# Optimization experiments

Hardware: AMD Instinct MI355X
Metric: run time of the kernel (lower is better)

## Reference

```python
import jax, jax.numpy as jnp
import numpy as np

B, N, DIM, HID, MAXN = 2048, 65536, 256, 512, 64
MID_KEY = (MAXN + HID) // 2   # 288
MID_VAL = (DIM + HID) // 2    # 384
MID_DEC = (HID + DIM) // 2    # 384
MID_SZ  = (HID + 1) // 2      # 256

def _ln(x, g, b):
    m = x.mean(-1, keepdims=True)
    v = ((x - m) ** 2).mean(-1, keepdims=True)
    return (x - m) * jax.lax.rsqrt(v + 1e-5) * g + b

def _mish(x):
    return x * jnp.tanh(jax.nn.softplus(x))

def _mlp_ln(x, W1, b1, g, be, W2, b2):
    return _mish(_ln(x @ W1 + b1, g, be)) @ W2 + b2

def _mlp(x, W1, b1, W2, b2):
    return _mish(x @ W1 + b1) @ W2 + b2

def setup_inputs():
    key = jax.random.key(0)
    ks = iter(jax.random.split(key, 40))
    def rn(shape, s=0.05):
        return jax.random.normal(next(ks), shape, jnp.float32) * s
    x = jax.random.normal(next(ks), (N, DIM), jnp.float32)
    batch = jnp.sort(jax.random.randint(next(ks), (N,), 0, B)).astype(jnp.int32)
    z32 = lambda *s: jnp.zeros(s, jnp.float32)
    o32 = lambda *s: jnp.ones(s, jnp.float32)
    return dict(
        x=x, batch=batch, n_batches=B,
        e_rank_W=rn((DIM, 1)), e_rank_b=z32(1),
        e_card_W=rn((1, HID)), e_card_b=z32(HID),
        e_key_W1=rn((MAXN, MID_KEY)), e_key_b1=z32(MID_KEY), e_key_g=o32(MID_KEY), e_key_be=z32(MID_KEY),
        e_key_W2=rn((MID_KEY, HID)), e_key_b2=z32(HID),
        e_val_W1=rn((DIM, MID_VAL)), e_val_b1=z32(MID_VAL), e_val_g=o32(MID_VAL), e_val_be=z32(MID_VAL),
        e_val_W2=rn((MID_VAL, HID)), e_val_b2=z32(HID),
        d_key_W1=rn((MAXN, MID_KEY)), d_key_b1=z32(MID_KEY), d_key_g=o32(MID_KEY), d_key_be=z32(MID_KEY),
        d_key_W2=rn((MID_KEY, HID)), d_key_b2=z32(HID),
        d_dec_W1=rn((HID, MID_DEC)), d_dec_b1=z32(MID_DEC),
        d_dec_W2=rn((MID_DEC, DIM)), d_dec_b2=z32(DIM),
        d_size_W1=rn((HID, MID_SZ)), d_size_b1=z32(MID_SZ), d_size_g=o32(MID_SZ), d_size_be=z32(MID_SZ),
        d_size_W2=rn((MID_SZ, 1)), d_size_b2=z32(1),
    )

def reference(x, batch, n_batches, e_rank_W, e_rank_b, e_card_W, e_card_b,
              e_key_W1, e_key_b1, e_key_g, e_key_be, e_key_W2, e_key_b2,
              e_val_W1, e_val_b1, e_val_g, e_val_be, e_val_W2, e_val_b2,
              d_key_W1, d_key_b1, d_key_g, d_key_be, d_key_W2, d_key_b2,
              d_dec_W1, d_dec_b1, d_dec_W2, d_dec_b2,
              d_size_W1, d_size_b1, d_size_g, d_size_be, d_size_W2, d_size_b2):
    max_n = e_key_W1.shape[0]
    n_pts = x.shape[0]
    # ---- Encoder ----
    n = jax.ops.segment_sum(jnp.ones(n_pts, jnp.float32), batch, num_segments=n_batches).astype(jnp.int32)
    mag = jnp.abs(x @ e_rank_W + e_rank_b)[:, 0]                 # [N]
    sort_key = batch.astype(jnp.float32) * jnp.max(mag) + mag    # sort within each set by |rank|
    idx = jnp.argsort(sort_key)
    xs = x[idx]
    starts = jnp.cumsum(n) - n                                   # per-set offsets (batch is sorted)
    pos_idx = jnp.arange(n_pts) - starts[batch]                  # rank within each set
    pos = jax.nn.one_hot(pos_idx, max_n, dtype=x.dtype)
    y = _mlp_ln(xs, e_val_W1, e_val_b1, e_val_g, e_val_be, e_val_W2, e_val_b2) \
      * _mlp_ln(pos, e_key_W1, e_key_b1, e_key_g, e_key_be, e_key_W2, e_key_b2)
    z = jax.ops.segment_sum(y, batch, num_segments=n_batches) \
      + n.astype(jnp.float32)[:, None] @ e_card_W + e_card_b     # [B, HID]
    # ---- Decoder ----
    n_logits = _mlp_ln(z, d_size_W1, d_size_b1, d_size_g, d_size_be, d_size_W2, d_size_b2)  # [B, 1]
    n_dec = jnp.clip(jnp.round(n_logits[:, 0]), 0, max_n).astype(jnp.int32)
    keys = _mlp_ln(jnp.eye(max_n, dtype=x.dtype),                # onehot positions 0..max_n-1
                   d_key_W1, d_key_b1, d_key_g, d_key_be, d_key_W2, d_key_b2)  # [max_n, HID]
    zp = z[:, None, :] * keys[None, :, :]                        # [B, max_n, HID] (repeat_interleave -> dense+mask)
    xf = _mlp(zp, d_dec_W1, d_dec_b1, d_dec_W2, d_dec_b2)        # [B, max_n, DIM]
    mask = jnp.arange(max_n)[None, :] < n_dec[:, None]           # valid rows per set
    x_out = (xf * mask[..., None].astype(xf.dtype)).reshape(-1, xf.shape[-1])
    batch_out = jnp.repeat(jnp.arange(n_batches, dtype=jnp.int32), max_n)
    return x_out, batch_out, mask.reshape(-1)
```

## Files before the change

kernel.cpp:

```cpp
#include <hip/hip_runtime.h>

#define NPTS   65536
#define NB     2048
#define DIMX   256
#define HIDN   512
#define MAXNN  64
#define MIDK   288
#define MIDV   384
#define MIDD   384
#define MIDS   256

typedef unsigned short ushort_t;
typedef __attribute__((ext_vector_type(8))) short short8;
typedef __attribute__((ext_vector_type(4))) float f32x4;

__device__ __forceinline__ float mishf(float x) {
    float e = __expf(fminf(x, 30.f));
    float n = e * (e + 2.f);
    return x * n * __builtin_amdgcn_rcpf(n + 2.f);
}
__device__ __forceinline__ ushort_t f2bf(float f) {
    unsigned u = __float_as_uint(f);
    u += 0x7fffu + ((u >> 16) & 1u);
    return (ushort_t)(u >> 16);
}
__device__ __forceinline__ float bf2f(ushort_t h) {
    return __uint_as_float(((unsigned)h) << 16);
}
__device__ __forceinline__ void dma16(const void* g, void* lds) {
    __builtin_amdgcn_global_load_lds(
        (const __attribute__((address_space(1))) unsigned int*)g,
        (__attribute__((address_space(3))) unsigned int*)lds, 16, 0, 0);
}

__global__ __launch_bounds__(256)
void k_starts(const int* __restrict__ batch, int* __restrict__ starts,
              unsigned int* __restrict__ maxmag, int* __restrict__ cnt)
{
    int b = blockIdx.x * blockDim.x + threadIdx.x;
    if (b == 0) { *maxmag = 0u; *cnt = 0; }
    if (b <= NB) {
        int lo = 0, hi = NPTS;
        while (lo < hi) { int mid = (lo + hi) >> 1; if (batch[mid] < b) lo = mid + 1; else hi = mid; }
        starts[b] = lo;
    }
}

__global__ __launch_bounds__(256)
void k_mag(const float* __restrict__ x, const float* __restrict__ rW,
           const float* __restrict__ rb, float* __restrict__ mag,
           unsigned int* __restrict__ maxmag, ushort_t* __restrict__ xb)
{
    const int lane = threadIdx.x & 63;
    const int wave = threadIdx.x >> 6;
    const int gw = blockIdx.x * 4 + wave;
    float4 wv = *(const float4*)(rW + lane * 4);
    float bias = rb[0];
    float lmax = 0.f;
    for (int pt = gw; pt < NPTS; pt += 16384) {
        float4 xv = *(const float4*)(x + (size_t)pt * DIMX + lane * 4);
        ushort4 u;
        u.x = f2bf(xv.x); u.y = f2bf(xv.y); u.z = f2bf(xv.z); u.w = f2bf(xv.w);
        *(ushort4*)(xb + (size_t)pt * DIMX + lane * 4) = u;
        double d = (double)xv.x * wv.x + (double)xv.y * wv.y
                 + (double)xv.z * wv.z + (double)xv.w * wv.w;
        #pragma unroll
        for (int o = 32; o > 0; o >>= 1) d += __shfl_xor(d, o);
        float s = fabsf((float)(d + (double)bias));
        if (lane == 0) mag[pt] = s;
        lmax = fmaxf(lmax, s);
    }
    __shared__ float wm[4];
    if (lane == 0) wm[wave] = lmax;
    __syncthreads();
    if (threadIdx.x == 0) {
        float m = fmaxf(fmaxf(wm[0], wm[1]), fmaxf(wm[2], wm[3]));
        atomicMax(maxmag, __float_as_uint(m));
    }
}

__global__ __launch_bounds__(256)
void k_rank(const int* __restrict__ batch, const int* __restrict__ starts,
            const float* __restrict__ mag, const unsigned int* __restrict__ maxmag,
            int* __restrict__ kidx)
{
    int i = blockIdx.x * 256 + threadIdx.x;
    if (i >= NPTS) return;
    int b = batch[i];
    int s = starts[b], e = starts[b + 1];
    float M = __uint_as_float(*maxmag);
    float kb = __fmul_rn((float)b, M);
    float ki = __fadd_rn(kb, mag[i]);
    int r = 0;
    for (int j = s; j < e; ++j) {
        float kj = __fadd_rn(kb, mag[j]);
        r += (kj < ki) || (kj == ki && j < i);
    }
    kidx[i] = (r < MAXNN) ? r : MAXNN;
}

__global__ __launch_bounds__(512)
void k_table(const float* __restrict__ W1, const float* __restrict__ b1,
             const float* __restrict__ g, const float* __restrict__ be,
             const float* __restrict__ W2, const float* __restrict__ b2,
             float* __restrict__ tbl, int in_dim, int n_w1_rows)
{
    const int row = blockIdx.x;
    const int t = threadIdx.x;
    __shared__ float h[MIDK];
    __shared__ float red[512];
    float v = 0.f;
    if (t < in_dim) v = b1[t] + (row < n_w1_rows ? W1[row * in_dim + t] : 0.f);
    red[t] = (t < in_dim) ? v : 0.f;
    __syncthreads();
    for (int o = 256; o > 0; o >>= 1) { if (t < o) red[t] += red[t + o]; __syncthreads(); }
    float m = red[0] / (float)in_dim;
    __syncthreads();
    float d = v - m;
    red[t] = (t < in_dim) ? d * d : 0.f;
    __syncthreads();
    for (int o = 256; o > 0; o >>= 1) { if (t < o) red[t] += red[t + o]; __syncthreads(); }
    float rs = rsqrtf(red[0] / (float)in_dim + 1e-5f);
    __syncthreads();
    if (t < in_dim) h[t] = mishf(d * rs * g[t] + be[t]);
    __syncthreads();
    float acc = b2[t];
    #pragma unroll 8
    for (int k = 0; k < MIDK; ++k) acc = fmaf(h[k], W2[k * HIDN + t], acc);
    tbl[row * HIDN + t] = acc;
}

__global__ __launch_bounds__(256)
void k_card(const int* __restrict__ starts, const float* __restrict__ cardW,
            const float* __restrict__ cardb, float* __restrict__ z)
{
    int idx = blockIdx.x * 256 + threadIdx.x;
    int b = idx >> 9, c = idx & 511;
    float n = (float)(starts[b + 1] - starts[b]);
    z[idx] = fmaf(n, cardW[c], cardb[c]);
}

__global__ __launch_bounds__(256)
void k_size(const float* __restrict__ z, const float* __restrict__ W1,
            const float* __restrict__ b1, const float* __restrict__ g,
            const float* __restrict__ be, const float* __restrict__ W2,
            const float* __restrict__ b2, int* __restrict__ ndec)
{
    const int b0 = blockIdx.x * 4, t = threadIdx.x;
    __shared__ float zr[4][HIDN];
    __shared__ float red[4][256];
    #pragma unroll
    for (int gI = 0; gI < 4; ++gI) {
        zr[gI][t] = z[(b0 + gI) * HIDN + t];
        zr[gI][t + 256] = z[(b0 + gI) * HIDN + 256 + t];
    }
    __syncthreads();
    float acc[4];
    float bb1 = b1[t];
    #pragma unroll
    for (int gI = 0; gI < 4; ++gI) acc[gI] = bb1;
    #pragma unroll 8
    for (int k = 0; k < HIDN; ++k) {
        float wv = W1[k * MIDS + t];
        #pragma unroll
        for (int gI = 0; gI < 4; ++gI) acc[gI] = fmaf(zr[gI][k], wv, acc[gI]);
    }
    #pragma unroll
    for (int gI = 0; gI < 4; ++gI) red[gI][t] = acc[gI];
    __syncthreads();
    for (int o = 128; o > 0; o >>= 1) {
        if (t < o) {
            #pragma unroll
            for (int gI = 0; gI < 4; ++gI) red[gI][t] += red[gI][t + o];
        }
        __syncthreads();
    }
    float mm[4];
    #pragma unroll
    for (int gI = 0; gI < 4; ++gI) mm[gI] = red[gI][0] * (1.f / 256.f);
    __syncthreads();
    #pragma unroll
    for (int gI = 0; gI < 4; ++gI) { float d = acc[gI] - mm[gI]; red[gI][t] = d * d; }
    __syncthreads();
    for (int o = 128; o > 0; o >>= 1) {
        if (t < o) {
            #pragma unroll
            for (int gI = 0; gI < 4; ++gI) red[gI][t] += red[gI][t + o];
        }
        __syncthreads();
    }
    float rs[4];
    #pragma unroll
    for (int gI = 0; gI < 4; ++gI) rs[gI] = rsqrtf(red[gI][0] * (1.f / 256.f) + 1e-5f);
    __syncthreads();
    float w2 = W2[t], gg = g[t], bbe = be[t];
    #pragma unroll
    for (int gI = 0; gI < 4; ++gI) {
        float h = mishf((acc[gI] - mm[gI]) * rs[gI] * gg + bbe);
        red[gI][t] = h * w2;
    }
    __syncthreads();
    for (int o = 128; o > 0; o >>= 1) {
        if (t < o) {
            #pragma unroll
            for (int gI = 0; gI < 4; ++gI) red[gI][t] += red[gI][t + o];
        }
        __syncthreads();
    }
    if (t < 4) {
        float logit = red[t][0] + b2[0];
        float n = rintf(logit);
        n = fminf(fmaxf(n, 0.f), 64.f);
        ndec[b0 + t] = (int)n;
    }
}

__global__ __launch_bounds__(256)
void k_compact(const int* __restrict__ ndec, int* __restrict__ cnt,
               int* __restrict__ rowmap)
{
    int b = blockIdx.x * 256 + threadIdx.x;
    if (b >= NB) return;
    int n = ndec[b];
    if (n > 0) {
        int base = atomicAdd(cnt, n);
        for (int p = 0; p < n; ++p) rowmap[base + p] = b * 64 + p;
    }
}

__global__ __launch_bounds__(128)
void k_pad(const int* __restrict__ cnt, int* __restrict__ cntpad,
           int* __restrict__ rowmap)
{
    int c = *cnt;
    int pad = (c + 127) & ~127;
    int t = threadIdx.x;
    if (c + t < pad) rowmap[c + t] = -1;
    if (t == 0) *cntpad = pad;
}

__global__ __launch_bounds__(256)
void k_tail(const int* __restrict__ ndec, float* __restrict__ outb,
            float* __restrict__ outm)
{
    int r = blockIdx.x * 256 + threadIdx.x;
    if (r < NB * MAXNN) {
        outb[r] = (float)(r >> 6);
        outm[r] = ((r & 63) < ndec[r >> 6]) ? 1.f : 0.f;
    }
}

__global__ __launch_bounds__(256)
void k_wt_all(const float* __restrict__ W0, ushort_t* __restrict__ T0,
              const float* __restrict__ W1s, ushort_t* __restrict__ T1,
              const float* __restrict__ W2s, ushort_t* __restrict__ T2,
              const float* __restrict__ W3s, ushort_t* __restrict__ T3)
{
    int idx = blockIdx.x * 256 + threadIdx.x;
    const float* W; ushort_t* T; int N, K, off;
    if (idx < 98304)       { W = W0;  T = T0; K = 256; N = 384; off = idx; }
    else if (idx < 294912) { W = W1s; T = T1; K = 384; N = 512; off = idx - 98304; }
    else if (idx < 491520) { W = W2s; T = T2; K = 512; N = 384; off = idx - 294912; }
    else                   { W = W3s; T = T3; K = 384; N = 256; off = idx - 491520; }
    int k = off / N, n = off - k * N;
    T[(size_t)n * K + k] = f2bf(W[off]);
}

__global__ __launch_bounds__(512, 2)
void k_mm_e1f(const ushort_t* __restrict__ A, const ushort_t* __restrict__ Bt,
              const float* __restrict__ bias, const float* __restrict__ g,
              const float* __restrict__ be, ushort_t* __restrict__ C)
{
    const int m0 = blockIdx.x * 128;
    __shared__ __align__(16) ushort_t As[128 * 64];
    __shared__ __align__(16) ushort_t Bs[384 * 64];
    const int t = threadIdx.x;
    const int l = t & 63;
    const int w = t >> 6;
    const int wm = (w >> 2) * 64;
    const int wq = (w & 3) * 96;
    const int l4 = (l >> 4) << 2;
    const int drow = l >> 3;
    const int dblk = (l & 7) ^ drow;

    f32x4 acc[4][6];
    #pragma unroll
    for (int a = 0; a < 4; ++a)
        #pragma unroll
        for (int b = 0; b < 6; ++b) acc[a][b] = (f32x4)0.f;

    for (int k0 = 0; k0 < DIMX; k0 += 64) {
        #pragma unroll
        for (int ii = 0; ii < 2; ++ii) {
            int i = w * 2 + ii;
            dma16(A + (size_t)(m0 + i * 8 + drow) * DIMX + k0 + dblk * 8, &As[i * 512]);
        }
        #pragma unroll
        for (int ii = 0; ii < 6; ++ii) {
            int i = w * 6 + ii;
            dma16(Bt + (size_t)(i * 8 + drow) * DIMX + k0 + dblk * 8, &Bs[i * 512]);
        }
        __syncthreads();
        #pragma unroll
        for (int ks = 0; ks < 2; ++ks) {
            int kq = ks * 4 + (l >> 4);
            short8 af[4], bfr[6];
            #pragma unroll
            for (int fm = 0; fm < 4; ++fm) {
                int row = wm + fm * 16 + (l & 15);
                af[fm] = *(const short8*)&As[row * 64 + ((kq ^ (row & 7)) << 3)];
            }
            #pragma unroll
            for (int fn = 0; fn < 6; ++fn) {
                int row = wq + fn * 16 + (l & 15);
                bfr[fn] = *(const short8*)&Bs[row * 64 + ((kq ^ (row & 7)) << 3)];
            }
            #pragma unroll
            for (int fm = 0; fm < 4; ++fm)
                #pragma unroll
                for (int fn = 0; fn < 6; ++fn)
                    acc[fm][fn] = __builtin_amdgcn_mfma_f32_16x16x32_bf16(
                        af[fm], bfr[fn], acc[fm][fn], 0, 0, 0);
        }
        __syncthreads();
    }

    float bb[6], gg[6], bee[6];
    #pragma unroll
    for (int fn = 0; fn < 6; ++fn) {
        int col = wq + fn * 16 + (l & 15);
        bb[fn] = bias[col]; gg[fn] = g[col]; bee[fn] = be[col];
    }
    #pragma unroll
    for (int fm = 0; fm < 4; ++fm)
        #pragma unroll
        for (int fn = 0; fn < 6; ++fn)
            #pragma unroll
            for (int j = 0; j < 4; ++j) acc[fm][fn][j] += bb[fn];

    float* ssum = (float*)As;
    float* ssq  = ssum + 512;
    #pragma unroll
    for (int fm = 0; fm < 4; ++fm) {
        #pragma unroll
        for (int j = 0; j < 4; ++j) {
            float s = 0.f, q = 0.f;
            #pragma unroll
            for (int fn = 0; fn < 6; ++fn) {
                float v = acc[fm][fn][j];
                s += v; q += v * v;
            }
            #pragma unroll
            for (int o = 1; o < 16; o <<= 1) {
                s += __shfl_xor(s, o);
                q += __shfl_xor(q, o);
            }
            if ((l & 15) == 0) {
                int r = wm + fm * 16 + l4 + j;
                ssum[r * 4 + (w & 3)] = s;
                ssq[r * 4 + (w & 3)] = q;
            }
        }
    }
    __syncthreads();
    #pragma unroll
    for (int fm = 0; fm < 4; ++fm) {
        #pragma unroll
        for (int j = 0; j < 4; ++j) {
            int r = wm + fm * 16 + l4 + j;
            float s = ssum[r * 4 + 0] + ssum[r * 4 + 1] + ssum[r * 4 + 2] + ssum[r * 4 + 3];
            float q = ssq[r * 4 + 0] + ssq[r * 4 + 1] + ssq[r * 4 + 2] + ssq[r * 4 + 3];
            float m = s * (1.f / 384.f);
            float var = q * (1.f / 384.f) - m * m;
            float rs = rsqrtf(var + 1e-5f);
            #pragma unroll
            for (int fn = 0; fn < 6; ++fn) {
                float v = (acc[fm][fn][j] - m) * rs * gg[fn] + bee[fn];
                C[(size_t)(m0 + r) * MIDV + wq + fn * 16 + (l & 15)] = f2bf(mishf(v));
            }
        }
    }
}

template<int MODE>
__device__ __forceinline__
void mm_body(const ushort_t* __restrict__ A, const ushort_t* __restrict__ Bt,
             const float* __restrict__ bias, void* __restrict__ Cptr, int K,
             const float* __restrict__ tbl, const int* __restrict__ kidx,
             const int* __restrict__ batch, float* __restrict__ zout,
             const float* __restrict__ zin, const int* __restrict__ rowmap,
             const int* __restrict__ cntpad)
{
    const int flat = blockIdx.y * gridDim.x + blockIdx.x;
    const int nx = gridDim.x;
    const int xcd = flat & 7;
    const int lin = flat >> 3;
    const int n0 = (lin % nx) * 128;
    const int m0 = ((lin / nx) + ((gridDim.y >> 3) * xcd)) * 128;
    if (MODE >= 2) {
        if (m0 >= *cntpad) return;
    }
    __shared__ __align__(16) ushort_t sAB[2 * 128 * 64];
    ushort_t* As = sAB;
    ushort_t* Bs = sAB + 128 * 64;
    const int t = threadIdx.x;
    const int l = t & 63;
    const int w = t >> 6;
    const int wm = (w >> 1) * 64;
    const int wn = (w & 1) * 64;
    const int l4 = (l >> 4) << 2;
    const int drow = l >> 3;
    const int dblk = (l & 7) ^ drow;

    int g4[4], p4[4];
    if (MODE == 2) {
        #pragma unroll
        for (int ii = 0; ii < 4; ++ii) {
            int i = w * 4 + ii;
            int gr = rowmap[m0 + i * 8 + drow];
            if (gr < 0) gr = 0;
            g4[ii] = gr >> 6; p4[ii] = gr & 63;
        }
    }

    f32x4 acc[4][4];
    #pragma unroll
    for (int a = 0; a < 4; ++a)
        #pragma unroll
        for (int b = 0; b < 4; ++b) acc[a][b] = (f32x4)0.f;

    for (int k0 = 0; k0 < K; k0 += 64) {
        if (MODE == 2) {
            #pragma unroll
            for (int ii = 0; ii < 4; ++ii) {
                int i = w * 4 + ii;
                int row = i * 8 + drow;
                const float* zp = zin + g4[ii] * HIDN + k0 + dblk * 8;
                const float* kp = tbl + p4[ii] * HIDN + k0 + dblk * 8;
                float4 z0 = *(const float4*)zp;
                float4 z1 = *(const float4*)(zp + 4);
                float4 q0 = *(const float4*)kp;
                float4 q1 = *(const float4*)(kp + 4);
                ushort4 u0, u1;
                u0.x = f2bf(z0.x * q0.x); u0.y = f2bf(z0.y * q0.y);
                u0.z = f2bf(z0.z * q0.z); u0.w = f2bf(z0.w * q0.w);
                u1.x = f2bf(z1.x * q1.x); u1.y = f2bf(z1.y * q1.y);
                u1.z = f2bf(z1.z * q1.z); u1.w = f2bf(z1.w * q1.w);
                ushort_t* dst = &As[row * 64 + (l & 7) * 8];
                *(ushort4*)dst = u0;
                *(ushort4*)(dst + 4) = u1;
            }
        } else {
            #pragma unroll
            for (int ii = 0; ii < 4; ++ii) {
                int i = w * 4 + ii;
                const ushort_t* g = A + (size_t)(m0 + i * 8 + drow) * K + k0 + dblk * 8;
                dma16(g, &As[i * 512]);
            }
        }
        #pragma unroll
        for (int ii = 0; ii < 4; ++ii) {
            int i = w * 4 + ii;
            const ushort_t* g = Bt + (size_t)(n0 + i * 8 + drow) * K + k0 + dblk * 8;
            dma16(g, &Bs[i * 512]);
        }
        __syncthreads();
        #pragma unroll
        for (int ks = 0; ks < 2; ++ks) {
            short8 af[4], bfr[4];
            int kq = ks * 4 + (l >> 4);
            #pragma unroll
            for (int fm = 0; fm < 4; ++fm) {
                int row = wm + fm * 16 + (l & 15);
                af[fm] = *(const short8*)&As[row * 64 + ((kq ^ (row & 7)) << 3)];
            }
            #pragma unroll
            for (int fn = 0; fn < 4; ++fn) {
                int row = wn + fn * 16 + (l & 15);
                bfr[fn] = *(const short8*)&Bs[row * 64 + ((kq ^ (row & 7)) << 3)];
            }
            #pragma unroll
            for (int fm = 0; fm < 4; ++fm)
                #pragma unroll
                for (int fn = 0; fn < 4; ++fn)
                    acc[fm][fn] = __builtin_amdgcn_mfma_f32_16x16x32_bf16(
                        af[fm], bfr[fn], acc[fm][fn], 0, 0, 0);
        }
        __syncthreads();
    }

    if (MODE == 1) {
        __shared__ int barr[128];
        __shared__ int karr[128];
        float* yred = (float*)sAB;
        if (t < 128) { barr[t] = batch[m0 + t]; karr[t] = kidx[m0 + t]; }
        __syncthreads();
        #pragma unroll
        for (int pass = 0; pass < 2; ++pass) {
            if (wm == pass * 64) {
                #pragma unroll
                for (int fn = 0; fn < 4; ++fn) {
                    int cl = wn + fn * 16 + (l & 15);
                    float bb = bias[n0 + cl];
                    #pragma unroll
                    for (int fm = 0; fm < 4; ++fm) {
                        #pragma unroll
                        for (int j = 0; j < 4; ++j) {
                            int rl = fm * 16 + l4 + j;
                            float v = (acc[fm][fn][j] + bb)
                                    * tbl[karr[pass * 64 + rl] * HIDN + (n0 + cl)];
                            yred[cl * 64 + (rl ^ (cl & 31))] = v;
                        }
                    }
                }
            }
            __syncthreads();
            {
                int c = t & 127, half = t >> 7;
                int gc = n0 + c;
                float run = 0.f; int curb = -1;
                #pragma unroll 1
                for (int rr = 0; rr < 32; ++rr) {
                    int rl = half * 32 + rr;
                    int b = barr[pass * 64 + rl];
                    float v = yred[c * 64 + (rl ^ (c & 31))];
                    if (b != curb) {
                        if (curb >= 0) atomicAdd(&zout[curb * HIDN + gc], run);
                        curb = b; run = v;
                    } else run += v;
                }
                atomicAdd(&zout[curb * HIDN + gc], run);
            }
            __syncthreads();
        }
    } else if (MODE == 2) {
        ushort_t* C = (ushort_t*)Cptr;
        #pragma unroll
        for (int fm = 0; fm < 4; ++fm) {
            int gr0 = m0 + wm + fm * 16 + l4;
            #pragma unroll
            for (int fn = 0; fn < 4; ++fn) {
                int gc = n0 + wn + fn * 16 + (l & 15);
                float bb = bias[gc];
                #pragma unroll
                for (int j = 0; j < 4; ++j)
                    C[(size_t)(gr0 + j) * MIDD + gc] = f2bf(mishf(acc[fm][fn][j] + bb));
            }
        }
    } else if (MODE == 3) {
        float* C = (float*)Cptr;
        #pragma unroll
        for (int fm = 0; fm < 4; ++fm) {
            int gr0 = m0 + wm + fm * 16 + l4;
            int om[4];
            #pragma unroll
            for (int j = 0; j < 4; ++j) om[j] = rowmap[gr0 + j];
            #pragma unroll
            for (int fn = 0; fn < 4; ++fn) {
                int gc = n0 + wn + fn * 16 + (l & 15);
                float bb = bias[gc];
                #pragma unroll
                for (int j = 0; j < 4; ++j)
                    if (om[j] >= 0) C[(size_t)om[j] * DIMX + gc] = acc[fm][fn][j] + bb;
            }
        }
    }
}

__global__ __launch_bounds__(256, 2)
void k_mm_e2(const ushort_t* A, const ushort_t* Bt, const float* bias, int K,
             const float* tbl, const int* kidx, const int* batch, float* zout)
{ mm_body<1>(A, Bt, bias, nullptr, K, tbl, kidx, batch, zout, nullptr, nullptr, nullptr); }

__global__ __launch_bounds__(256, 2)
void k_mm_d1(const ushort_t* Bt, const float* bias, void* C, int K,
             const float* tbl, const float* zin, const int* rowmap, const int* cntpad)
{ mm_body<2>(nullptr, Bt, bias, C, K, tbl, nullptr, nullptr, nullptr, zin, rowmap, cntpad); }

__global__ __launch_bounds__(256, 2)
void k_mm_d2(const ushort_t* A, const ushort_t* Bt, const float* bias, void* C, int K,
             const int* rowmap, const int* cntpad)
{ mm_body<3>(A, Bt, bias, C, K, nullptr, nullptr, nullptr, nullptr, nullptr, rowmap, cntpad); }

extern "C" void kernel_launch(void* const* d_in, const int* in_sizes, int n_in,
                              void* d_out, int out_size, void* d_ws, size_t ws_size,
                              hipStream_t stream)
{
    const float* x        = (const float*)d_in[0];
    const int*   batch    = (const int*)  d_in[1];
    const float* e_rank_W = (const float*)d_in[3];
    const float* e_rank_b = (const float*)d_in[4];
    const float* e_card_W = (const float*)d_in[5];
    const float* e_card_b = (const float*)d_in[6];
    const float* e_key_W1 = (const float*)d_in[7];
    const float* e_key_b1 = (const float*)d_in[8];
    const float* e_key_g  = (const float*)d_in[9];
    const float* e_key_be = (const float*)d_in[10];
    const float* e_key_W2 = (const float*)d_in[11];
    const float* e_key_b2 = (const float*)d_in[12];
    const float* e_val_W1 = (const float*)d_in[13];
    const float* e_val_b1 = (const float*)d_in[14];
    const float* e_val_g  = (const float*)d_in[15];
    const float* e_val_be = (const float*)d_in[16];
    const float* e_val_W2 = (const float*)d_in[17];
    const float* e_val_b2 = (const float*)d_in[18];
    const float* d_key_W1 = (const float*)d_in[19];
    const float* d_key_b1 = (const float*)d_in[20];
    const float* d_key_g  = (const float*)d_in[21];
    const float* d_key_be = (const float*)d_in[22];
    const float* d_key_W2 = (const float*)d_in[23];
    const float* d_key_b2 = (const float*)d_in[24];
    const float* d_dec_W1 = (const float*)d_in[25];
    const float* d_dec_b1 = (const float*)d_in[26];
    const float* d_dec_W2 = (const float*)d_in[27];
    const float* d_dec_b2 = (const float*)d_in[28];
    const float* d_size_W1= (const float*)d_in[29];
    const float* d_size_b1= (const float*)d_in[30];
    const float* d_size_g = (const float*)d_in[31];
    const float* d_size_be= (const float*)d_in[32];
    const float* d_size_W2= (const float*)d_in[33];
    const float* d_size_b2= (const float*)d_in[34];

    char* ws = (char*)d_ws;
    int*          starts  = (int*)         (ws + 0);
    unsigned int* maxmag  = (unsigned int*)(ws + 8448);
    int*          kidx    = (int*)         (ws + 8704);
    float*        mag     = (float*)       (ws + 270848);
    float*        enc_tbl = (float*)       (ws + 532992);
    float*        dec_tbl = (float*)       (ws + 666112);
    float*        z       = (float*)       (ws + 797184);
    int*          ndec    = (int*)         (ws + 4991488);
    int*          cnt     = (int*)         (ws + 4999680);
    int*          cntpad  = (int*)         (ws + 4999684);
    int*          rowmap  = (int*)         (ws + 5000192);
    ushort_t*     evW1t   = (ushort_t*)    (ws + 5524480);
    ushort_t*     evW2t   = (ushort_t*)    (ws + 5721088);
    ushort_t*     ddW1t   = (ushort_t*)    (ws + 6114304);
    ushort_t*     ddW2t   = (ushort_t*)    (ws + 6507520);
    ushort_t*     xb      = (ushort_t*)    (ws + 6704384);
    ushort_t*     Hb      = (ushort_t*)    (ws + 6704384 + 33554432);
    ushort_t*     Hd      = (ushort_t*)    (ws + 6704384);

    float* out_x = (float*)d_out;
    float* out_b = out_x + (size_t)NB * MAXNN * DIMX;
    float* out_m = out_b + NB * MAXNN;

    hipMemsetAsync(out_x, 0, (size_t)NB * MAXNN * DIMX * sizeof(float), stream);
    k_starts<<<dim3(9), dim3(256), 0, stream>>>(batch, starts, maxmag, cnt);
    k_mag<<<dim3(4096), dim3(256), 0, stream>>>(x, e_rank_W, e_rank_b, mag, maxmag, xb);
    k_rank<<<dim3(256), dim3(256), 0, stream>>>(batch, starts, mag, maxmag, kidx);
    k_table<<<dim3(65), dim3(512), 0, stream>>>(e_key_W1, e_key_b1, e_key_g, e_key_be,
                                                e_key_W2, e_key_b2, enc_tbl, MIDK, 64);
    k_table<<<dim3(64), dim3(512), 0, stream>>>(d_key_W1, d_key_b1, d_key_g, d_key_be,
                                                d_key_W2, d_key_b2, dec_tbl, MIDK, 64);
    k_card<<<dim3(4096), dim3(256), 0, stream>>>(starts, e_card_W, e_card_b, z);
    k_wt_all<<<dim3(2304), dim3(256), 0, stream>>>(e_val_W1, evW1t, e_val_W2, evW2t,
                                                   d_dec_W1, ddW1t, d_dec_W2, ddW2t);

    k_mm_e1f<<<dim3(512), dim3(512), 0, stream>>>(xb, evW1t, e_val_b1,
                                                  e_val_g, e_val_be, Hb);
    k_mm_e2<<<dim3(4, 512), dim3(256), 0, stream>>>(Hb, evW2t, e_val_b2, MIDV,
                                                    enc_tbl, kidx, batch, z);
    k_size<<<dim3(NB / 4), dim3(256), 0, stream>>>(z, d_size_W1, d_size_b1, d_size_g,
                                                   d_size_be, d_size_W2, d_size_b2, ndec);
    k_compact<<<dim3(8), dim3(256), 0, stream>>>(ndec, cnt, rowmap);
    k_pad<<<dim3(1), dim3(128), 0, stream>>>(cnt, cntpad, rowmap);
    k_mm_d1<<<dim3(3, 1024), dim3(256), 0, stream>>>(ddW1t, d_dec_b1, Hd, HIDN,
                                                     dec_tbl, z, rowmap, cntpad);
    k_mm_d2<<<dim3(2, 1024), dim3(256), 0, stream>>>(Hd, ddW2t, d_dec_b2, out_x, MIDD,
                                                     rowmap, cntpad);
    k_tail<<<dim3(512), dim3(256), 0, stream>>>(ndec, out_b, out_m);
}
```

Measured before the change: 520.6 us.

## Fuse encoder value MLP GEMMs and merge small setup kernels

Fuses the two encoder value-MLP GEMMs into one kernel. The bf16 hidden activations stay in LDS, laid out as swizzled K-panels, instead of round-tripping a 65536x384 buffer through global memory. The second GEMM loops over four 128-column output tiles per block, reusing the resident hidden slab, and performs the key-table multiply and segment-sum atomics in the epilogue. It also merges the two key-table launches into one grid and replaces the compact and pad kernels with a single-block kernel using an LDS counter. The cost is about 129 KB of LDS per block, which limits occupancy, and a serialized loop over output tiles within each block.

```diff
diff --git a/kernel.cpp b/kernel.cpp
--- a/kernel.cpp
+++ b/kernel.cpp
@@ -35,10 +35,10 @@
 
 __global__ __launch_bounds__(256)
 void k_starts(const int* __restrict__ batch, int* __restrict__ starts,
-              unsigned int* __restrict__ maxmag, int* __restrict__ cnt)
+              unsigned int* __restrict__ maxmag)
 {
     int b = blockIdx.x * blockDim.x + threadIdx.x;
-    if (b == 0) { *maxmag = 0u; *cnt = 0; }
+    if (b == 0) *maxmag = 0u;
     if (b <= NB) {
         int lo = 0, hi = NPTS;
         while (lo < hi) { int mid = (lo + hi) >> 1; if (batch[mid] < b) lo = mid + 1; else hi = mid; }
@@ -100,34 +100,46 @@
 }
 
 __global__ __launch_bounds__(512)
-void k_table(const float* __restrict__ W1, const float* __restrict__ b1,
-             const float* __restrict__ g, const float* __restrict__ be,
-             const float* __restrict__ W2, const float* __restrict__ b2,
-             float* __restrict__ tbl, int in_dim, int n_w1_rows)
+void k_table2(const float* __restrict__ eW1, const float* __restrict__ eb1,
+              const float* __restrict__ eg, const float* __restrict__ ebe,
+              const float* __restrict__ eW2, const float* __restrict__ eb2,
+              const float* __restrict__ dW1, const float* __restrict__ db1,
+              const float* __restrict__ dg, const float* __restrict__ dbe,
+              const float* __restrict__ dW2, const float* __restrict__ db2,
+              float* __restrict__ enc_tbl, float* __restrict__ dec_tbl)
 {
     const int row = blockIdx.x;
     const int t = threadIdx.x;
+    const float *W1, *b1, *g, *be, *W2, *b2; float* out; int wrow;
+    if (row < 65) {
+        W1 = eW1; b1 = eb1; g = eg; be = ebe; W2 = eW2; b2 = eb2;
+        out = enc_tbl + row * HIDN; wrow = (row < 64) ? row : -1;
+    } else {
+        int r = row - 65;
+        W1 = dW1; b1 = db1; g = dg; be = dbe; W2 = dW2; b2 = db2;
+        out = dec_tbl + r * HIDN; wrow = r;
+    }
     __shared__ float h[MIDK];
     __shared__ float red[512];
     float v = 0.f;
-    if (t < in_dim) v = b1[t] + (row < n_w1_rows ? W1[row * in_dim + t] : 0.f);
-    red[t] = (t < in_dim) ? v : 0.f;
+    if (t < MIDK) v = b1[t] + (wrow >= 0 ? W1[wrow * MIDK + t] : 0.f);
+    red[t] = (t < MIDK) ? v : 0.f;
     __syncthreads();
     for (int o = 256; o > 0; o >>= 1) { if (t < o) red[t] += red[t + o]; __syncthreads(); }
-    float m = red[0] / (float)in_dim;
+    float m = red[0] / (float)MIDK;
     __syncthreads();
     float d = v - m;
-    red[t] = (t < in_dim) ? d * d : 0.f;
+    red[t] = (t < MIDK) ? d * d : 0.f;
     __syncthreads();
     for (int o = 256; o > 0; o >>= 1) { if (t < o) red[t] += red[t + o]; __syncthreads(); }
-    float rs = rsqrtf(red[0] / (float)in_dim + 1e-5f);
-    __syncthreads();
-    if (t < in_dim) h[t] = mishf(d * rs * g[t] + be[t]);
+    float rs = rsqrtf(red[0] / (float)MIDK + 1e-5f);
+    __syncthreads();
+    if (t < MIDK) h[t] = mishf(d * rs * g[t] + be[t]);
     __syncthreads();
     float acc = b2[t];
     #pragma unroll 8
     for (int k = 0; k < MIDK; ++k) acc = fmaf(h[k], W2[k * HIDN + t], acc);
-    tbl[row * HIDN + t] = acc;
+    out[t] = acc;
 }
 
 __global__ __launch_bounds__(256)
@@ -216,26 +228,24 @@
 }
 
 __global__ __launch_bounds__(256)
-void k_compact(const int* __restrict__ ndec, int* __restrict__ cnt,
-               int* __restrict__ rowmap)
-{
-    int b = blockIdx.x * 256 + threadIdx.x;
-    if (b >= NB) return;
-    int n = ndec[b];
-    if (n > 0) {
-        int base = atomicAdd(cnt, n);
-        for (int p = 0; p < n; ++p) rowmap[base + p] = b * 64 + p;
-    }
-}
-
-__global__ __launch_bounds__(128)
-void k_pad(const int* __restrict__ cnt, int* __restrict__ cntpad,
-           int* __restrict__ rowmap)
-{
-    int c = *cnt;
+void k_compact_pad(const int* __restrict__ ndec, int* __restrict__ rowmap,
+                   int* __restrict__ cntpad)
+{
+    __shared__ int lcnt;
+    const int t = threadIdx.x;
+    if (t == 0) lcnt = 0;
+    __syncthreads();
+    for (int b = t; b < NB; b += 256) {
+        int n = ndec[b];
+        if (n > 0) {
+            int base = atomicAdd(&lcnt, n);
+            for (int p = 0; p < n; ++p) rowmap[base + p] = b * 64 + p;
+        }
+    }
+    __syncthreads();
+    int c = lcnt;
     int pad = (c + 127) & ~127;
-    int t = threadIdx.x;
-    if (c + t < pad) rowmap[c + t] = -1;
+    for (int i = c + t; i < pad; i += 256) rowmap[i] = -1;
     if (t == 0) *cntpad = pad;
 }
 
@@ -267,22 +277,34 @@
 }
 
 __global__ __launch_bounds__(512, 2)
-void k_mm_e1f(const ushort_t* __restrict__ A, const ushort_t* __restrict__ Bt,
-              const float* __restrict__ bias, const float* __restrict__ g,
-              const float* __restrict__ be, ushort_t* __restrict__ C)
+void k_enc(const ushort_t* __restrict__ A, const ushort_t* __restrict__ B1t,
+           const float* __restrict__ b1, const float* __restrict__ g,
+           const float* __restrict__ be, const ushort_t* __restrict__ B2t,
+           const float* __restrict__ b2, const float* __restrict__ tbl,
+           const int* __restrict__ kidx, const int* __restrict__ batch,
+           float* __restrict__ zout)
 {
     const int m0 = blockIdx.x * 128;
-    __shared__ __align__(16) ushort_t As[128 * 64];
-    __shared__ __align__(16) ushort_t Bs[384 * 64];
+    __shared__ __align__(16) char SMEM[132096];
+    ushort_t* slab = (ushort_t*)SMEM;
+    ushort_t* As   = slab;
+    ushort_t* Bs   = slab + 8192;
+    ushort_t* Bs2  = (ushort_t*)(SMEM + 98304);
+    float*    yred = (float*)(SMEM + 98304);
+    float*    ssum = (float*)(SMEM + 98304);
+    float*    ssq  = ssum + 512;
+    int*      barr = (int*)(SMEM + 131072);
+    int*      karr = barr + 128;
+
     const int t = threadIdx.x;
     const int l = t & 63;
     const int w = t >> 6;
-    const int wm = (w >> 2) * 64;
-    const int wq = (w & 3) * 96;
     const int l4 = (l >> 4) << 2;
     const int drow = l >> 3;
     const int dblk = (l & 7) ^ drow;
 
+    const int wmA = (w >> 2) * 64;
+    const int wqA = (w & 3) * 96;
     f32x4 acc[4][6];
     #pragma unroll
     for (int a = 0; a < 4; ++a)
@@ -298,7 +320,7 @@
         #pragma unroll
         for (int ii = 0; ii < 6; ++ii) {
             int i = w * 6 + ii;
-            dma16(Bt + (size_t)(i * 8 + drow) * DIMX + k0 + dblk * 8, &Bs[i * 512]);
+            dma16(B1t + (size_t)(i * 8 + drow) * DIMX + k0 + dblk * 8, &Bs[i * 512]);
         }
         __syncthreads();
         #pragma unroll
@@ -307,12 +329,12 @@
             short8 af[4], bfr[6];
             #pragma unroll
             for (int fm = 0; fm < 4; ++fm) {
-                int row = wm + fm * 16 + (l & 15);
+                int row = wmA + fm * 16 + (l & 15);
                 af[fm] = *(const short8*)&As[row * 64 + ((kq ^ (row & 7)) << 3)];
             }
             #pragma unroll
             for (int fn = 0; fn < 6; ++fn) {
-                int row = wq + fn * 16 + (l & 15);
+                int row = wqA + fn * 16 + (l & 15);
                 bfr[fn] = *(const short8*)&Bs[row * 64 + ((kq ^ (row & 7)) << 3)];
             }
             #pragma unroll
@@ -328,8 +350,8 @@
     float bb[6], gg[6], bee[6];
     #pragma unroll
     for (int fn = 0; fn < 6; ++fn) {
-        int col = wq + fn * 16 + (l & 15);
-        bb[fn] = bias[col]; gg[fn] = g[col]; bee[fn] = be[col];
+        int col = wqA + fn * 16 + (l & 15);
+        bb[fn] = b1[col]; gg[fn] = g[col]; bee[fn] = be[col];
     }
     #pragma unroll
     for (int fm = 0; fm < 4; ++fm)
@@ -338,8 +360,6 @@
             #pragma unroll
             for (int j = 0; j < 4; ++j) acc[fm][fn][j] += bb[fn];
 
-    float* ssum = (float*)As;
-    float* ssq  = ssum + 512;
     #pragma unroll
     for (int fm = 0; fm < 4; ++fm) {
         #pragma unroll
@@ -356,18 +376,20 @@
                 q += __shfl_xor(q, o);
             }
             if ((l & 15) == 0) {
-                int r = wm + fm * 16 + l4 + j;
+                int r = wmA + fm * 16 + l4 + j;
                 ssum[r * 4 + (w & 3)] = s;
                 ssq[r * 4 + (w & 3)] = q;
             }
         }
     }
-    __syncthreads();
+    if (t < 128) { barr[t] = batch[m0 + t]; karr[t] = kidx[m0 + t]; }
+    __syncthreads();
+
     #pragma unroll
     for (int fm = 0; fm < 4; ++fm) {
         #pragma unroll
         for (int j = 0; j < 4; ++j) {
-            int r = wm + fm * 16 + l4 + j;
+            int r = wmA + fm * 16 + l4 + j;
             float s = ssum[r * 4 + 0] + ssum[r * 4 + 1] + ssum[r * 4 + 2] + ssum[r * 4 + 3];
             float q = ssq[r * 4 + 0] + ssq[r * 4 + 1] + ssq[r * 4 + 2] + ssq[r * 4 + 3];
             float m = s * (1.f / 384.f);
@@ -376,8 +398,98 @@
             #pragma unroll
             for (int fn = 0; fn < 6; ++fn) {
                 float v = (acc[fm][fn][j] - m) * rs * gg[fn] + bee[fn];
-                C[(size_t)(m0 + r) * MIDV + wq + fn * 16 + (l & 15)] = f2bf(mishf(v));
-            }
+                int c = wqA + fn * 16 + (l & 15);
+                int panel = c >> 6, cc = c & 63;
+                int kb = (cc >> 3) ^ (r & 7);
+                slab[panel * 8192 + r * 64 + kb * 8 + (cc & 7)] = f2bf(mishf(v));
+            }
+        }
+    }
+    __syncthreads();
+
+    const int wmB = (w >> 1) * 32;
+    const int wnB = (w & 1) * 64;
+    for (int nt = 0; nt < 4; ++nt) {
+        const int n0t = nt * 128;
+        f32x4 acc2[2][4];
+        #pragma unroll
+        for (int a = 0; a < 2; ++a)
+            #pragma unroll
+            for (int b = 0; b < 4; ++b) acc2[a][b] = (f32x4)0.f;
+
+        for (int k0 = 0; k0 < MIDV; k0 += 64) {
+            const int panel = k0 >> 6;
+            #pragma unroll
+            for (int ii = 0; ii < 2; ++ii) {
+                int i = w * 2 + ii;
+                dma16(B2t + (size_t)(n0t + i * 8 + drow) * MIDV + k0 + dblk * 8,
+                      &Bs2[i * 512]);
+            }
+            __syncthreads();
+            #pragma unroll
+            for (int ks = 0; ks < 2; ++ks) {
+                int kq = ks * 4 + (l >> 4);
+                short8 af[2], bfr[4];
+                #pragma unroll
+                for (int fm = 0; fm < 2; ++fm) {
+                    int row = wmB + fm * 16 + (l & 15);
+                    af[fm] = *(const short8*)&slab[panel * 8192 + row * 64
+                                                   + ((kq ^ (row & 7)) << 3)];
+                }
+                #pragma unroll
+                for (int fn = 0; fn < 4; ++fn) {
+                    int row = wnB + fn * 16 + (l & 15);
+                    bfr[fn] = *(const short8*)&Bs2[row * 64 + ((kq ^ (row & 7)) << 3)];
+                }
+                #pragma unroll
+                for (int fm = 0; fm < 2; ++fm)
+                    #pragma unroll
+                    for (int fn = 0; fn < 4; ++fn)
+                        acc2[fm][fn] = __builtin_amdgcn_mfma_f32_16x16x32_bf16(
+                            af[fm], bfr[fn], acc2[fm][fn], 0, 0, 0);
+            }
+            __syncthreads();
+        }
+
+        #pragma unroll
+        for (int ph = 0; ph < 2; ++ph) {
+            if ((w >> 2) == ph) {
+                int rowbase = ((w >> 1) & 1) * 32;
+                #pragma unroll
+                for (int fn = 0; fn < 4; ++fn) {
+                    int cl = wnB + fn * 16 + (l & 15);
+                    float bbv = b2[n0t + cl];
+                    #pragma unroll
+                    for (int fm = 0; fm < 2; ++fm) {
+                        #pragma unroll
+                        for (int j = 0; j < 4; ++j) {
+                            int rl = rowbase + fm * 16 + l4 + j;
+                            int rg = ph * 64 + rl;
+                            float v = (acc2[fm][fn][j] + bbv)
+                                    * tbl[karr[rg] * HIDN + n0t + cl];
+                            yred[cl * 64 + (rl ^ (cl & 31))] = v;
+                        }
+                    }
+                }
+            }
+            __syncthreads();
+            {
+                int c = t & 127, q4 = t >> 7;
+                int gc = n0t + c;
+                float run = 0.f; int curb = -1;
+                #pragma unroll 1
+                for (int rr = 0; rr < 16; ++rr) {
+                    int rl = q4 * 16 + rr;
+                    int b = barr[ph * 64 + rl];
+                    float v = yred[c * 64 + (rl ^ (c & 31))];
+                    if (b != curb) {
+                        if (curb >= 0) atomicAdd(&zout[curb * HIDN + gc], run);
+                        curb = b; run = v;
+                    } else run += v;
+                }
+                atomicAdd(&zout[curb * HIDN + gc], run);
+            }
+            __syncthreads();
         }
     }
 }
@@ -386,10 +498,8 @@
 __device__ __forceinline__
 void mm_body(const ushort_t* __restrict__ A, const ushort_t* __restrict__ Bt,
              const float* __restrict__ bias, void* __restrict__ Cptr, int K,
-             const float* __restrict__ tbl, const int* __restrict__ kidx,
-             const int* __restrict__ batch, float* __restrict__ zout,
-             const float* __restrict__ zin, const int* __restrict__ rowmap,
-             const int* __restrict__ cntpad)
+             const float* __restrict__ tbl, const float* __restrict__ zin,
+             const int* __restrict__ rowmap, const int* __restrict__ cntpad)
 {
     const int flat = blockIdx.y * gridDim.x + blockIdx.x;
     const int nx = gridDim.x;
@@ -397,9 +507,7 @@
     const int lin = flat >> 3;
     const int n0 = (lin % nx) * 128;
     const int m0 = ((lin / nx) + ((gridDim.y >> 3) * xcd)) * 128;
-    if (MODE >= 2) {
-        if (m0 >= *cntpad) return;
-    }
+    if (m0 >= *cntpad) return;
     __shared__ __align__(16) ushort_t sAB[2 * 128 * 64];
     ushort_t* As = sAB;
     ushort_t* Bs = sAB + 128 * 64;
@@ -454,15 +562,15 @@
             #pragma unroll
             for (int ii = 0; ii < 4; ++ii) {
                 int i = w * 4 + ii;
-                const ushort_t* g = A + (size_t)(m0 + i * 8 + drow) * K + k0 + dblk * 8;
-                dma16(g, &As[i * 512]);
+                const ushort_t* gp = A + (size_t)(m0 + i * 8 + drow) * K + k0 + dblk * 8;
+                dma16(gp, &As[i * 512]);
             }
         }
         #pragma unroll
         for (int ii = 0; ii < 4; ++ii) {
             int i = w * 4 + ii;
-            const ushort_t* g = Bt + (size_t)(n0 + i * 8 + drow) * K + k0 + dblk * 8;
-            dma16(g, &Bs[i * 512]);
+            const ushort_t* gp = Bt + (size_t)(n0 + i * 8 + drow) * K + k0 + dblk * 8;
+            dma16(gp, &Bs[i * 512]);
         }
         __syncthreads();
         #pragma unroll
@@ -489,51 +597,7 @@
         __syncthreads();
     }
 
-    if (MODE == 1) {
-        __shared__ int barr[128];
-        __shared__ int karr[128];
-        float* yred = (float*)sAB;
-        if (t < 128) { barr[t] = batch[m0 + t]; karr[t] = kidx[m0 + t]; }
-        __syncthreads();
-        #pragma unroll
-        for (int pass = 0; pass < 2; ++pass) {
-            if (wm == pass * 64) {
-                #pragma unroll
-                for (int fn = 0; fn < 4; ++fn) {
-                    int cl = wn + fn * 16 + (l & 15);
-                    float bb = bias[n0 + cl];
-                    #pragma unroll
-                    for (int fm = 0; fm < 4; ++fm) {
-                        #pragma unroll
-                        for (int j = 0; j < 4; ++j) {
-                            int rl = fm * 16 + l4 + j;
-                            float v = (acc[fm][fn][j] + bb)
-                                    * tbl[karr[pass * 64 + rl] * HIDN + (n0 + cl)];
-                            yred[cl * 64 + (rl ^ (cl & 31))] = v;
-                        }
-                    }
-                }
-            }
-            __syncthreads();
-            {
-                int c = t & 127, half = t >> 7;
-                int gc = n0 + c;
-                float run = 0.f; int curb = -1;
-                #pragma unroll 1
-                for (int rr = 0; rr < 32; ++rr) {
-                    int rl = half * 32 + rr;
-                    int b = barr[pass * 64 + rl];
-                    float v = yred[c * 64 + (rl ^ (c & 31))];
-                    if (b != curb) {
-                        if (curb >= 0) atomicAdd(&zout[curb * HIDN + gc], run);
-                        curb = b; run = v;
-                    } else run += v;
-                }
-                atomicAdd(&zout[curb * HIDN + gc], run);
-            }
-            __syncthreads();
-        }
-    } else if (MODE == 2) {
+    if (MODE == 2) {
         ushort_t* C = (ushort_t*)Cptr;
         #pragma unroll
         for (int fm = 0; fm < 4; ++fm) {
@@ -541,13 +605,13 @@
             #pragma unroll
             for (int fn = 0; fn < 4; ++fn) {
                 int gc = n0 + wn + fn * 16 + (l & 15);
-                float bb = bias[gc];
+                float bbv = bias[gc];
                 #pragma unroll
                 for (int j = 0; j < 4; ++j)
-                    C[(size_t)(gr0 + j) * MIDD + gc] = f2bf(mishf(acc[fm][fn][j] + bb));
-            }
-        }
-    } else if (MODE == 3) {
+                    C[(size_t)(gr0 + j) * MIDD + gc] = f2bf(mishf(acc[fm][fn][j] + bbv));
+            }
+        }
+    } else {
         float* C = (float*)Cptr;
         #pragma unroll
         for (int fm = 0; fm < 4; ++fm) {
@@ -558,29 +622,24 @@
             #pragma unroll
             for (int fn = 0; fn < 4; ++fn) {
                 int gc = n0 + wn + fn * 16 + (l & 15);
-                float bb = bias[gc];
+                float bbv = bias[gc];
                 #pragma unroll
                 for (int j = 0; j < 4; ++j)
-                    if (om[j] >= 0) C[(size_t)om[j] * DIMX + gc] = acc[fm][fn][j] + bb;
-            }
-        }
-    }
-}
-
-__global__ __launch_bounds__(256, 2)
-void k_mm_e2(const ushort_t* A, const ushort_t* Bt, const float* bias, int K,
-             const float* tbl, const int* kidx, const int* batch, float* zout)
-{ mm_body<1>(A, Bt, bias, nullptr, K, tbl, kidx, batch, zout, nullptr, nullptr, nullptr); }
+                    if (om[j] >= 0) C[(size_t)om[j] * DIMX + gc] = acc[fm][fn][j] + bbv;
+            }
+        }
+    }
+}
 
 __global__ __launch_bounds__(256, 2)
 void k_mm_d1(const ushort_t* Bt, const float* bias, void* C, int K,
              const float* tbl, const float* zin, const int* rowmap, const int* cntpad)
-{ mm_body<2>(nullptr, Bt, bias, C, K, tbl, nullptr, nullptr, nullptr, zin, rowmap, cntpad); }
+{ mm_body<2>(nullptr, Bt, bias, C, K, tbl, zin, rowmap, cntpad); }
 
 __global__ __launch_bounds__(256, 2)
 void k_mm_d2(const ushort_t* A, const ushort_t* Bt, const float* bias, void* C, int K,
              const int* rowmap, const int* cntpad)
-{ mm_body<3>(A, Bt, bias, C, K, nullptr, nullptr, nullptr, nullptr, nullptr, rowmap, cntpad); }
+{ mm_body<3>(A, Bt, bias, C, K, nullptr, nullptr, rowmap, cntpad); }
 
 extern "C" void kernel_launch(void* const* d_in, const int* in_sizes, int n_in,
                               void* d_out, int out_size, void* d_ws, size_t ws_size,
@@ -630,7 +689,6 @@
     float*        dec_tbl = (float*)       (ws + 666112);
     float*        z       = (float*)       (ws + 797184);
     int*          ndec    = (int*)         (ws + 4991488);
-    int*          cnt     = (int*)         (ws + 4999680);
     int*          cntpad  = (int*)         (ws + 4999684);
     int*          rowmap  = (int*)         (ws + 5000192);
     ushort_t*     evW1t   = (ushort_t*)    (ws + 5524480);
@@ -638,33 +696,30 @@
     ushort_t*     ddW1t   = (ushort_t*)    (ws + 6114304);
     ushort_t*     ddW2t   = (ushort_t*)    (ws + 6507520);
     ushort_t*     xb      = (ushort_t*)    (ws + 6704384);
-    ushort_t*     Hb      = (ushort_t*)    (ws + 6704384 + 33554432);
-    ushort_t*     Hd      = (ushort_t*)    (ws + 6704384);
+    ushort_t*     Hd      = (ushort_t*)    (ws + 6704384 + 33554432);
 
     float* out_x = (float*)d_out;
     float* out_b = out_x + (size_t)NB * MAXNN * DIMX;
     float* out_m = out_b + NB * MAXNN;
 
     hipMemsetAsync(out_x, 0, (size_t)NB * MAXNN * DIMX * sizeof(float), stream);
-    k_starts<<<dim3(9), dim3(256), 0, stream>>>(batch, starts, maxmag, cnt);
+    k_starts<<<dim3(9), dim3(256), 0, stream>>>(batch, starts, maxmag);
     k_mag<<<dim3(4096), dim3(256), 0, stream>>>(x, e_rank_W, e_rank_b, mag, maxmag, xb);
     k_rank<<<dim3(256), dim3(256), 0, stream>>>(batch, starts, mag, maxmag, kidx);
-    k_table<<<dim3(65), dim3(512), 0, stream>>>(e_key_W1, e_key_b1, e_key_g, e_key_be,
-                                                e_key_W2, e_key_b2, enc_tbl, MIDK, 64);
-    k_table<<<dim3(64), dim3(512), 0, stream>>>(d_key_W1, d_key_b1, d_key_g, d_key_be,
-                                                d_key_W2, d_key_b2, dec_tbl, MIDK, 64);
+    k_table2<<<dim3(129), dim3(512), 0, stream>>>(
+        e_key_W1, e_key_b1, e_key_g, e_key_be, e_key_W2, e_key_b2,
+        d_key_W1, d_key_b1, d_key_g, d_key_be, d_key_W2, d_key_b2,
+        enc_tbl, dec_tbl);
     k_card<<<dim3(4096), dim3(256), 0, stream>>>(starts, e_card_W, e_card_b, z);
     k_wt_all<<<dim3(2304), dim3(256), 0, stream>>>(e_val_W1, evW1t, e_val_W2, evW2t,
                                                    d_dec_W1, ddW1t, d_dec_W2, ddW2t);
 
-    k_mm_e1f<<<dim3(512), dim3(512), 0, stream>>>(xb, evW1t, e_val_b1,
-                                                  e_val_g, e_val_be, Hb);
-    k_mm_e2<<<dim3(4, 512), dim3(256), 0, stream>>>(Hb, evW2t, e_val_b2, MIDV,
-                                                    enc_tbl, kidx, batch, z);
+    k_enc<<<dim3(512), dim3(512), 0, stream>>>(xb, evW1t, e_val_b1, e_val_g, e_val_be,
+                                               evW2t, e_val_b2, enc_tbl, kidx, batch, z);
+
     k_size<<<dim3(NB / 4), dim3(256), 0, stream>>>(z, d_size_W1, d_size_b1, d_size_g,
                                                    d_size_be, d_size_W2, d_size_b2, ndec);
-    k_compact<<<dim3(8), dim3(256), 0, stream>>>(ndec, cnt, rowmap);
-    k_pad<<<dim3(1), dim3(128), 0, stream>>>(cnt, cntpad, rowmap);
+    k_compact_pad<<<dim3(1), dim3(256), 0, stream>>>(ndec, rowmap, cntpad);
     k_mm_d1<<<dim3(3, 1024), dim3(256), 0, stream>>>(ddW1t, d_dec_b1, Hd, HIDN,
                                                      dec_tbl, z, rowmap, cntpad);
     k_mm_d2<<<dim3(2, 1024), dim3(256), 0, stream>>>(Hd, ddW2t, d_dec_b2, out_x, MIDD,
```

After: 523.3 us. Within noise of the previous version (+0.5%).
